# Kernel tuning notes

Measured on AMD Instinct MI355X. Metric: run time of the kernel, lower is better.

Reference implementation:

```python
import jax, jax.numpy as jnp
import numpy as np
from jax import lax

NT, TL = 32, 64           # num_trajs, traj_length
H, W, C = 84, 84, 4       # Atari frame stack
SIZE = 256                # LSTM hidden size
NOUT = 18                 # num_outputs
FEAT = 6 * 6 * 32         # after four stride-2 SAME convs: 84->42->21->11->6
DN = ('NHWC', 'HWIO', 'NHWC')


def setup_inputs() -> dict:
    key = jax.random.key(0)
    ks = jax.random.split(key, 8)
    d = {}
    d['inputs'] = jax.random.normal(ks[0], (NT * TL, H, W, C), jnp.float32)
    cin = C
    for i in range(4):
        d[f'w{i+1}'] = jax.random.normal(ks[1 + i], (3, 3, cin, 32), jnp.float32) * 0.1
        d[f'b{i+1}'] = jnp.zeros((32,), jnp.float32)
        cin = 32
    d['lstm_w'] = jax.random.normal(ks[5], (FEAT + SIZE, 4 * SIZE), jnp.float32) * 0.05
    d['lstm_b'] = jnp.zeros((4 * SIZE,), jnp.float32)
    d['fc_w'] = jax.random.normal(ks[6], (SIZE, NOUT), jnp.float32) * 0.01
    d['fc_b'] = jnp.zeros((NOUT,), jnp.float32)
    d['c0'] = jnp.zeros((NT, SIZE), jnp.float32)
    d['h0'] = jnp.zeros((NT, SIZE), jnp.float32)
    return d


def reference(inputs, w1, b1, w2, b2, w3, b3, w4, b4,
              lstm_w, lstm_b, fc_w, fc_b, c0, h0):
    x = inputs
    for w, b in ((w1, b1), (w2, b2), (w3, b3), (w4, b4)):
        x = jax.nn.elu(lax.conv_general_dilated(
            x, w, window_strides=(2, 2), padding='SAME',
            dimension_numbers=DN) + b)
    # [NT*TL, 6, 6, 32] -> [TL, NT, FEAT] (time-major for scan)
    xs = x.reshape(NT, TL, FEAT).transpose(1, 0, 2)

    def step(carry, xt):
        c, h = carry
        gates = jnp.concatenate([xt, h], axis=-1) @ lstm_w + lstm_b
        i, j, f, o = jnp.split(gates, 4, axis=-1)
        # BasicLSTMCell with forget_bias = 1.0
        new_c = c * jax.nn.sigmoid(f + 1.0) + jax.nn.sigmoid(i) * jnp.tanh(j)
        new_h = jnp.tanh(new_c) * jax.nn.sigmoid(o)
        return (new_c, new_h), new_h

    _, outs = lax.scan(step, (c0, h0), xs)          # outs: [TL, NT, SIZE]
    feats = outs.transpose(1, 0, 2).reshape(-1, SIZE)  # batch-major flatten
    logits = feats @ fc_w + fc_b                    # [NT*TL, NOUT]
    return logits
```

## Files before the change

kernel.cpp:

```cpp
#include <hip/hip_runtime.h>
#include <math.h>

#define NTRAJ 32
#define TLEN  64
#define BATCH (NTRAJ*TLEN)

__device__ __forceinline__ float eluf(float x){ return x > 0.f ? x : expm1f(x); }
__device__ __forceinline__ float sigmf(float x){ return 1.f/(1.f+expf(-x)); }

__global__ __launch_bounds__(256) void conv1_kernel(
    const float* __restrict__ in,
    const float* __restrict__ w,
    const float* __restrict__ b,
    float* __restrict__ out)
{
    int bid = blockIdx.x;
    bid = (bid & 7)*1764 + (bid >> 3);
    int pos = bid*256 + threadIdx.x;
    int n   = pos / (42*42);
    int rem = pos % (42*42);
    int oy  = rem / 42, ox = rem % 42;
    float acc[32];
    #pragma unroll
    for(int o=0;o<32;o++) acc[o] = b[o];
    for(int ky=0; ky<3; ky++){
        int iy = 2*oy + ky;
        if(iy >= 84) continue;
        for(int kx=0; kx<3; kx++){
            int ix = 2*ox + kx;
            if(ix >= 84) continue;
            float4 v = *(const float4*)(in + (((n*84 + iy)*84) + ix)*4);
            const float* wq = w + (ky*3 + kx)*128;
            #pragma unroll
            for(int o=0;o<32;o++) acc[o] += v.x*wq[o];
            #pragma unroll
            for(int o=0;o<32;o++) acc[o] += v.y*wq[32+o];
            #pragma unroll
            for(int o=0;o<32;o++) acc[o] += v.z*wq[64+o];
            #pragma unroll
            for(int o=0;o<32;o++) acc[o] += v.w*wq[96+o];
        }
    }
    float4* op = (float4*)(out + (size_t)pos*32);
    #pragma unroll
    for(int q=0;q<8;q++)
        op[q] = make_float4(eluf(acc[4*q]), eluf(acc[4*q+1]),
                            eluf(acc[4*q+2]), eluf(acc[4*q+3]));
}

template<int IH, int IW, int OH, int OW, int PB>
__global__ __launch_bounds__(256) void convN_kernel(
    const float* __restrict__ in,
    const float* __restrict__ w,
    const float* __restrict__ b,
    float* __restrict__ out)
{
    int bid = blockIdx.x;
    const int cpx = gridDim.x >> 3;
    bid = (bid & 7)*cpx + (bid >> 3);
    int pos = bid*256 + threadIdx.x;
    if(pos >= BATCH*OH*OW) return;
    int n   = pos / (OH*OW);
    int rem = pos % (OH*OW);
    int oy  = rem / OW, ox = rem % OW;
    float acc[32];
    #pragma unroll
    for(int o=0;o<32;o++) acc[o] = b[o];
    for(int ky=0; ky<3; ky++){
        int iy = 2*oy + ky - PB;
        if(iy < 0 || iy >= IH) continue;
        for(int kx=0; kx<3; kx++){
            int ix = 2*ox + kx - PB;
            if(ix < 0 || ix >= IW) continue;
            const float4* ip = (const float4*)(in + ((size_t)(n*IH + iy)*IW + ix)*32);
            const float* wp = w + (ky*3 + kx)*1024;
            #pragma unroll
            for(int c4=0;c4<8;c4++){
                float4 x = ip[c4];
                const float* wq = wp + c4*128;
                #pragma unroll
                for(int o=0;o<32;o++) acc[o] += x.x*wq[o];
                #pragma unroll
                for(int o=0;o<32;o++) acc[o] += x.y*wq[32+o];
                #pragma unroll
                for(int o=0;o<32;o++) acc[o] += x.z*wq[64+o];
                #pragma unroll
                for(int o=0;o<32;o++) acc[o] += x.w*wq[96+o];
            }
        }
    }
    float4* op = (float4*)(out + (size_t)pos*32);
    #pragma unroll
    for(int q=0;q<8;q++)
        op[q] = make_float4(eluf(acc[4*q]), eluf(acc[4*q+1]),
                            eluf(acc[4*q+2]), eluf(acc[4*q+3]));
}

__global__ __launch_bounds__(256) void relayout_kernel(
    const float* __restrict__ p4,
    float* __restrict__ at,
    unsigned long long* __restrict__ hbuf)
{
    int i = blockIdx.x*256 + threadIdx.x;
    if(i < 64*8192) hbuf[i] = 0ull;
    int f = i >> 11, r = i & 2047;
    int tt = r >> 5, n = r & 31;
    int nt = n*64 + tt;
    at[i] = p4[nt*1152 + f];
}

__global__ __launch_bounds__(256) void gx_gemm_kernel(
    const float* __restrict__ at,
    const float* __restrict__ lw,
    const float* __restrict__ lb,
    float* __restrict__ gx)
{
    int lane = threadIdx.x & 63;
    int wv   = threadIdx.x >> 6;
    int r0   = blockIdx.x * 16;
    int oc   = blockIdx.y*256 + wv*64 + lane;
    float acc[16];
    float bias = lb[oc];
    #pragma unroll
    for(int i=0;i<16;i++) acc[i] = bias;
    #pragma unroll 4
    for(int k=0;k<1152;k++){
        float wval = lw[k*1024 + oc];
        const float* ap = at + k*2048 + r0;
        #pragma unroll
        for(int i=0;i<16;i++) acc[i] += ap[i] * wval;
    }
    #pragma unroll
    for(int i=0;i<16;i++) gx[(r0+i)*1024 + oc] = acc[i];
}

__global__ __launch_bounds__(256) void lstm_coop_kernel(
    const float* __restrict__ gx,
    const float* __restrict__ lw,
    const float* __restrict__ c0,
    const float* __restrict__ h0,
    float* __restrict__ feats,
    unsigned long long* __restrict__ hbuf)
{
    __shared__ float hs[32*260];
    __shared__ float wp[16*516];
    __shared__ float gl[32*33];

    const int wg = blockIdx.x;
    const int t  = threadIdx.x;
    const float* wh = lw + 1152*1024;

    for(int i=0;i<32;i++){
        int e = t + 256*i;
        int k = e >> 5, c = e & 31;
        int gc = (c>>3)*256 + wg*8 + (c&7);
        wp[(c>>1)*516 + (k>>1)*4 + (k&1)*2 + (c&1)] = wh[k*1024 + gc];
    }
    const int un = t >> 3, uu = t & 7;
    float cst = c0[un*256 + wg*8 + uu];

    const int np = t >> 4, cp = t & 15;
    const int n0 = 2*np, n1 = 2*np + 1;
    const int c0l = 2*cp, c1l = 2*cp + 1;
    const int g0 = (c0l>>3)*256 + wg*8 + (c0l&7);
    const int g1 = (c1l>>3)*256 + wg*8 + (c1l&7);

    const float4* hs4 = (const float4*)hs;
    const float4* wp4 = (const float4*)wp;
    __syncthreads();

    for(int st=0; st<64; ++st){
        const float* gr0 = gx + (size_t)(st*32 + n0)*1024;
        const float* gr1 = gx + (size_t)(st*32 + n1)*1024;
        float gx00 = gr0[g0], gx01 = gr0[g1];
        float gx10 = gr1[g0], gx11 = gr1[g1];

        if(st == 0){
            const float4* hp4 = (const float4*)h0;
            #pragma unroll
            for(int i=0;i<8;i++){
                int q = t + 256*i;
                int row = q >> 6, col4 = q & 63;
                ((float4*)hs)[row*65 + col4] = hp4[q];
            }
        } else {
            const unsigned long long* src = hbuf + (size_t)(st-1)*8192;
            const unsigned tag = (unsigned)st;
            unsigned long long v[32];
            #pragma unroll
            for(int i=0;i<32;i++)
                v[i] = __hip_atomic_load(&src[i*256 + t],
                    __ATOMIC_RELAXED, __HIP_MEMORY_SCOPE_AGENT);
            unsigned spins = 0;
            for(;;){
                bool ok = true;
                #pragma unroll
                for(int i=0;i<32;i++){
                    if((unsigned)(v[i] >> 32) != tag){
                        v[i] = __hip_atomic_load(&src[i*256 + t],
                            __ATOMIC_RELAXED, __HIP_MEMORY_SCOPE_AGENT);
                        ok = false;
                    }
                }
                if(ok) break;
                __builtin_amdgcn_s_sleep(1);
                if(++spins > (1u<<21)) break;
            }
            #pragma unroll
            for(int i=0;i<32;i++)
                hs[i*260 + t] = __uint_as_float((unsigned)v[i]);
        }
        __syncthreads();

        float a00=0.f, a01=0.f, a10=0.f, a11=0.f;
        const float4* h0r = hs4 + n0*65;
        const float4* h1r = hs4 + n1*65;
        const float4* wr  = wp4 + cp*129;
        #pragma unroll 8
        for(int k4=0;k4<64;k4++){
            float4 A = wr[2*k4], B = wr[2*k4+1];
            float4 x = h0r[k4], y = h1r[k4];
            a00 += x.x*A.x + x.y*A.z + x.z*B.x + x.w*B.z;
            a01 += x.x*A.y + x.y*A.w + x.z*B.y + x.w*B.w;
            a10 += y.x*A.x + y.y*A.z + y.z*B.x + y.w*B.z;
            a11 += y.x*A.y + y.y*A.w + y.z*B.y + y.w*B.w;
        }
        gl[n0*33 + c0l] = a00 + gx00;
        gl[n0*33 + c1l] = a01 + gx01;
        gl[n1*33 + c0l] = a10 + gx10;
        gl[n1*33 + c1l] = a11 + gx11;
        __syncthreads();

        {
            float i_ = gl[un*33 +      uu];
            float j_ = gl[un*33 +  8 + uu];
            float f_ = gl[un*33 + 16 + uu];
            float o_ = gl[un*33 + 24 + uu];
            cst = cst*sigmf(f_ + 1.f) + sigmf(i_)*tanhf(j_);
            float h = tanhf(cst)*sigmf(o_);
            int col = wg*8 + uu;
            feats[(un*64 + st)*256 + col] = h;
            unsigned long long pv =
                ((unsigned long long)(unsigned)(st+1) << 32) |
                (unsigned long long)__float_as_uint(h);
            __hip_atomic_store(&hbuf[(size_t)st*8192 + un*256 + col], pv,
                               __ATOMIC_RELAXED, __HIP_MEMORY_SCOPE_AGENT);
        }
        __syncthreads();
    }
}

__global__ __launch_bounds__(64) void fc_kernel(
    const float* __restrict__ feats, const float* __restrict__ fw,
    const float* __restrict__ fb,    float* __restrict__ out)
{
    __shared__ float h[256];
    int p = blockIdx.x, t = threadIdx.x;
    *(float4*)&h[t*4] = *(const float4*)(feats + p*256 + t*4);
    __syncthreads();
    if(t < 18){
        float acc = fb[t];
        for(int k=0;k<256;k++) acc += h[k]*fw[k*18 + t];
        out[p*18 + t] = acc;
    }
}

extern "C" void kernel_launch(void* const* d_in, const int* in_sizes, int n_in,
                              void* d_out, int out_size, void* d_ws, size_t ws_size,
                              hipStream_t stream) {
    const float* inp = (const float*)d_in[0];
    const float* w1  = (const float*)d_in[1];  const float* b1 = (const float*)d_in[2];
    const float* w2  = (const float*)d_in[3];  const float* b2 = (const float*)d_in[4];
    const float* w3  = (const float*)d_in[5];  const float* b3 = (const float*)d_in[6];
    const float* w4  = (const float*)d_in[7];  const float* b4 = (const float*)d_in[8];
    const float* lw  = (const float*)d_in[9];  const float* lb = (const float*)d_in[10];
    const float* fw  = (const float*)d_in[11]; const float* fb = (const float*)d_in[12];
    const float* c0  = (const float*)d_in[13]; const float* h0 = (const float*)d_in[14];
    float* out = (float*)d_out;
    float* ws  = (float*)d_ws;

    const size_t n1 = (size_t)32*3612672;
    const size_t n3 = (size_t)32*247808;
    const size_t n4 = (size_t)32*73728;

    float* p1 = ws;
    float* p2 = p1 + n1;
    float* p3 = ws;
    float* p4 = p3 + n3;
    float* at = p4 + n4;
    float* gxb   = at  + (size_t)1152*2048;
    float* feats = gxb + (size_t)2048*1024;
    unsigned long long* hbuf =
        (unsigned long long*)(feats + (size_t)2048*256);

    conv1_kernel<<<14112,256,0,stream>>>(inp, w1, b1, p1);
    convN_kernel<42,42,21,21,0><<<3528,256,0,stream>>>(p1, w2, b2, p2);
    convN_kernel<21,21,11,11,1><<<968,256,0,stream>>>(p2, w3, b3, p3);
    convN_kernel<11,11, 6, 6,1><<<288,256,0,stream>>>(p3, w4, b4, p4);
    relayout_kernel<<<9216,256,0,stream>>>(p4, at, hbuf);
    gx_gemm_kernel<<<dim3(128,4),256,0,stream>>>(at, lw, lb, gxb);
    lstm_coop_kernel<<<32,256,0,stream>>>(gxb, lw, c0, h0, feats, hbuf);
    fc_kernel<<<2048,64,0,stream>>>(feats, fw, fb, out);
}
```

Measured before the change: 1.784 ms.

## Stage conv input tiles in shared memory and enlarge gx GEMM row tile

All four conv kernels now load an image row-band (or whole images for the later layers) into shared memory in channel-planar layout once per block. Each thread then reads its 3x3 window from LDS instead of re-reading overlapping input pixels from global memory, so the grids are retiled per image or tile. The gx GEMM now handles 32 rows per block instead of 16, which reuses each weight load more at the cost of extra registers. Risks include lower occupancy from the larger LDS footprint and idle threads in the partially filled tiles.

```diff
diff --git a/kernel.cpp b/kernel.cpp
--- a/kernel.cpp
+++ b/kernel.cpp
@@ -14,86 +14,139 @@
     const float* __restrict__ b,
     float* __restrict__ out)
 {
+    constexpr int IH=84, IW=84, OH=42, OW=42;
+    constexpr int SROWS=25, NPX=SROWS*IW, NPXP=NPX+1;
+    __shared__ float xs[4*NPXP];
     int bid = blockIdx.x;
-    bid = (bid & 7)*1764 + (bid >> 3);
-    int pos = bid*256 + threadIdx.x;
-    int n   = pos / (42*42);
-    int rem = pos % (42*42);
-    int oy  = rem / 42, ox = rem % 42;
-    float acc[32];
-    #pragma unroll
-    for(int o=0;o<32;o++) acc[o] = b[o];
-    for(int ky=0; ky<3; ky++){
-        int iy = 2*oy + ky;
-        if(iy >= 84) continue;
-        for(int kx=0; kx<3; kx++){
-            int ix = 2*ox + kx;
-            if(ix >= 84) continue;
-            float4 v = *(const float4*)(in + (((n*84 + iy)*84) + ix)*4);
-            const float* wq = w + (ky*3 + kx)*128;
-            #pragma unroll
-            for(int o=0;o<32;o++) acc[o] += v.x*wq[o];
-            #pragma unroll
-            for(int o=0;o<32;o++) acc[o] += v.y*wq[32+o];
-            #pragma unroll
-            for(int o=0;o<32;o++) acc[o] += v.z*wq[64+o];
-            #pragma unroll
-            for(int o=0;o<32;o++) acc[o] += v.w*wq[96+o];
-        }
-    }
-    float4* op = (float4*)(out + (size_t)pos*32);
-    #pragma unroll
-    for(int q=0;q<8;q++)
-        op[q] = make_float4(eluf(acc[4*q]), eluf(acc[4*q+1]),
-                            eluf(acc[4*q+2]), eluf(acc[4*q+3]));
-}
-
-template<int IH, int IW, int OH, int OW, int PB>
-__global__ __launch_bounds__(256) void convN_kernel(
+    bid = (bid & 7)*(8192/8) + (bid >> 3);
+    const int img  = bid >> 2;
+    const int tile = bid & 3;
+    const int oy0  = tile*12;
+    const int R    = (tile==3) ? 6 : 12;
+    const int iy0  = 2*oy0;
+    const int rows = min(SROWS, IH - iy0);
+    const int t = threadIdx.x;
+    const float4* gs = (const float4*)(in + (((size_t)img*IH + iy0)*IW)*4);
+    for(int p = t; p < rows*IW; p += 256){
+        float4 v = gs[p];
+        xs[0*NPXP + p] = v.x;  xs[1*NPXP + p] = v.y;
+        xs[2*NPXP + p] = v.z;  xs[3*NPXP + p] = v.w;
+    }
+    __syncthreads();
+    const int npo = R*OW;
+    if(t < 252){
+        for(int h=0; h<2; ++h){
+            int px = t + h*252;
+            if(px >= npo) break;
+            int oy = oy0 + px/OW, ox = px%OW;
+            float acc[32];
+            #pragma unroll
+            for(int o=0;o<32;o++) acc[o] = b[o];
+            for(int ky=0;ky<3;ky++){
+                int iy = 2*oy + ky;
+                if(iy >= IH) continue;
+                int rb = (iy - iy0)*IW;
+                for(int kx=0;kx<3;kx++){
+                    int ix = 2*ox + kx;
+                    if(ix >= IW) continue;
+                    const float* wq = w + (ky*3 + kx)*128;
+                    float x0 = xs[0*NPXP + rb + ix];
+                    float x1 = xs[1*NPXP + rb + ix];
+                    float x2 = xs[2*NPXP + rb + ix];
+                    float x3 = xs[3*NPXP + rb + ix];
+                    #pragma unroll
+                    for(int o=0;o<32;o++) acc[o] += x0*wq[o];
+                    #pragma unroll
+                    for(int o=0;o<32;o++) acc[o] += x1*wq[32+o];
+                    #pragma unroll
+                    for(int o=0;o<32;o++) acc[o] += x2*wq[64+o];
+                    #pragma unroll
+                    for(int o=0;o<32;o++) acc[o] += x3*wq[96+o];
+                }
+            }
+            float4* op = (float4*)(out + ((size_t)(img*OH + oy)*OW + ox)*32);
+            #pragma unroll
+            for(int q=0;q<8;q++)
+                op[q] = make_float4(eluf(acc[4*q]), eluf(acc[4*q+1]),
+                                    eluf(acc[4*q+2]), eluf(acc[4*q+3]));
+        }
+    }
+}
+
+template<int IH,int IW,int OH,int OW,int PB,int NIMG,int OROWS,int NTILES>
+__global__ __launch_bounds__(256) void convT_kernel(
     const float* __restrict__ in,
     const float* __restrict__ w,
     const float* __restrict__ b,
     float* __restrict__ out)
 {
+    constexpr int SROWS = (NTILES==1) ? IH : (2*OROWS+1);
+    constexpr int NPX   = NIMG*SROWS*IW;
+    constexpr int NPXP  = NPX + ((NPX&1) ? 0 : 1);
+    __shared__ float xs[32*NPXP];
     int bid = blockIdx.x;
-    const int cpx = gridDim.x >> 3;
-    bid = (bid & 7)*cpx + (bid >> 3);
-    int pos = bid*256 + threadIdx.x;
-    if(pos >= BATCH*OH*OW) return;
-    int n   = pos / (OH*OW);
-    int rem = pos % (OH*OW);
-    int oy  = rem / OW, ox = rem % OW;
-    float acc[32];
-    #pragma unroll
-    for(int o=0;o<32;o++) acc[o] = b[o];
-    for(int ky=0; ky<3; ky++){
-        int iy = 2*oy + ky - PB;
-        if(iy < 0 || iy >= IH) continue;
-        for(int kx=0; kx<3; kx++){
-            int ix = 2*ox + kx - PB;
-            if(ix < 0 || ix >= IW) continue;
-            const float4* ip = (const float4*)(in + ((size_t)(n*IH + iy)*IW + ix)*32);
-            const float* wp = w + (ky*3 + kx)*1024;
-            #pragma unroll
-            for(int c4=0;c4<8;c4++){
-                float4 x = ip[c4];
-                const float* wq = wp + c4*128;
-                #pragma unroll
-                for(int o=0;o<32;o++) acc[o] += x.x*wq[o];
-                #pragma unroll
-                for(int o=0;o<32;o++) acc[o] += x.y*wq[32+o];
-                #pragma unroll
-                for(int o=0;o<32;o++) acc[o] += x.z*wq[64+o];
-                #pragma unroll
-                for(int o=0;o<32;o++) acc[o] += x.w*wq[96+o];
+    bid = (bid & 7)*(gridDim.x >> 3) + (bid >> 3);
+    const int img0 = (bid / NTILES)*NIMG;
+    const int tile = bid % NTILES;
+    const int oy0  = tile*OROWS;
+    const int R    = min(OROWS, OH - oy0);
+    const int iy0  = (NTILES==1) ? 0 : 2*oy0;
+    const int rows = min(SROWS, IH - iy0);
+    const int t = threadIdx.x;
+    for(int il=0; il<NIMG; ++il){
+        const float4* gs = (const float4*)(in + (((size_t)(img0+il)*IH + iy0)*IW)*32);
+        const int ne = rows*IW*8;
+        for(int e=t; e<ne; e+=256){
+            int px = e >> 3, c4 = e & 7;
+            float4 v = gs[e];
+            int bb = il*(SROWS*IW) + px;
+            xs[(c4*4+0)*NPXP + bb] = v.x;
+            xs[(c4*4+1)*NPXP + bb] = v.y;
+            xs[(c4*4+2)*NPXP + bb] = v.z;
+            xs[(c4*4+3)*NPXP + bb] = v.w;
+        }
+    }
+    __syncthreads();
+    const int npo = NIMG*R*OW;
+    if(t < npo){
+        const int il  = t/(R*OW);
+        const int rem = t%(R*OW);
+        const int oy  = oy0 + rem/OW;
+        const int ox  = rem%OW;
+        float acc[32];
+        #pragma unroll
+        for(int o=0;o<32;o++) acc[o] = b[o];
+        for(int ky=0;ky<3;ky++){
+            int iy = 2*oy + ky - PB;
+            if(iy < iy0 || iy >= IH) continue;
+            for(int kx=0;kx<3;kx++){
+                int ix = 2*ox + kx - PB;
+                if(ix < 0 || ix >= IW) continue;
+                int base = il*(SROWS*IW) + (iy-iy0)*IW + ix;
+                const float* wp = w + (ky*3 + kx)*1024;
+                for(int ci=0;ci<32;ci+=4){
+                    float x0 = xs[(ci+0)*NPXP + base];
+                    float x1 = xs[(ci+1)*NPXP + base];
+                    float x2 = xs[(ci+2)*NPXP + base];
+                    float x3 = xs[(ci+3)*NPXP + base];
+                    const float* wq = wp + ci*32;
+                    #pragma unroll
+                    for(int o=0;o<32;o++) acc[o] += x0*wq[o];
+                    #pragma unroll
+                    for(int o=0;o<32;o++) acc[o] += x1*wq[32+o];
+                    #pragma unroll
+                    for(int o=0;o<32;o++) acc[o] += x2*wq[64+o];
+                    #pragma unroll
+                    for(int o=0;o<32;o++) acc[o] += x3*wq[96+o];
+                }
             }
         }
-    }
-    float4* op = (float4*)(out + (size_t)pos*32);
-    #pragma unroll
-    for(int q=0;q<8;q++)
-        op[q] = make_float4(eluf(acc[4*q]), eluf(acc[4*q+1]),
-                            eluf(acc[4*q+2]), eluf(acc[4*q+3]));
+        float4* op = (float4*)(out + ((size_t)((img0+il)*OH + oy)*OW + ox)*32);
+        #pragma unroll
+        for(int q=0;q<8;q++)
+            op[q] = make_float4(eluf(acc[4*q]), eluf(acc[4*q+1]),
+                                eluf(acc[4*q+2]), eluf(acc[4*q+3]));
+    }
 }
 
 __global__ __launch_bounds__(256) void relayout_kernel(
@@ -117,21 +170,21 @@
 {
     int lane = threadIdx.x & 63;
     int wv   = threadIdx.x >> 6;
-    int r0   = blockIdx.x * 16;
+    int r0   = blockIdx.x * 32;
     int oc   = blockIdx.y*256 + wv*64 + lane;
-    float acc[16];
+    float acc[32];
     float bias = lb[oc];
     #pragma unroll
-    for(int i=0;i<16;i++) acc[i] = bias;
-    #pragma unroll 4
+    for(int i=0;i<32;i++) acc[i] = bias;
+    #pragma unroll 2
     for(int k=0;k<1152;k++){
         float wval = lw[k*1024 + oc];
         const float* ap = at + k*2048 + r0;
         #pragma unroll
-        for(int i=0;i<16;i++) acc[i] += ap[i] * wval;
+        for(int i=0;i<32;i++) acc[i] += ap[i] * wval;
     }
     #pragma unroll
-    for(int i=0;i<16;i++) gx[(r0+i)*1024 + oc] = acc[i];
+    for(int i=0;i<32;i++) gx[(r0+i)*1024 + oc] = acc[i];
 }
 
 __global__ __launch_bounds__(256) void lstm_coop_kernel(
@@ -293,12 +346,12 @@
     unsigned long long* hbuf =
         (unsigned long long*)(feats + (size_t)2048*256);
 
-    conv1_kernel<<<14112,256,0,stream>>>(inp, w1, b1, p1);
-    convN_kernel<42,42,21,21,0><<<3528,256,0,stream>>>(p1, w2, b2, p2);
-    convN_kernel<21,21,11,11,1><<<968,256,0,stream>>>(p2, w3, b3, p3);
-    convN_kernel<11,11, 6, 6,1><<<288,256,0,stream>>>(p3, w4, b4, p4);
+    conv1_kernel<<<8192,256,0,stream>>>(inp, w1, b1, p1);
+    convT_kernel<42,42,21,21,0,1, 6,4><<<8192,256,0,stream>>>(p1, w2, b2, p2);
+    convT_kernel<21,21,11,11,1,1,11,1><<<2048,256,0,stream>>>(p2, w3, b3, p3);
+    convT_kernel<11,11, 6, 6,1,4, 6,1><<< 512,256,0,stream>>>(p3, w4, b4, p4);
     relayout_kernel<<<9216,256,0,stream>>>(p4, at, hbuf);
-    gx_gemm_kernel<<<dim3(128,4),256,0,stream>>>(at, lw, lb, gxb);
+    gx_gemm_kernel<<<dim3(64,4),256,0,stream>>>(at, lw, lb, gxb);
     lstm_coop_kernel<<<32,256,0,stream>>>(gxb, lw, c0, h0, feats, hbuf);
     fc_kernel<<<2048,64,0,stream>>>(feats, fw, fb, out);
 }
```

Result: slower. 2.423 ms (+35.8%).

## Compute two adjacent output pixels per thread in conv kernels, widen GEMM tile

Applied to the files above, without the earlier changes.

Each conv thread now computes two horizontally adjacent output pixels. It loads a 5-wide input row strip once, so the overlapping input column is reused and each weight load feeds two FMAs. This halves weight-load traffic per FMA and cuts grid sizes, at the cost of doubled accumulator registers and possibly lower occupancy. The gx GEMM also processes 32 rows per block instead of 16 to reuse each weight value more.

```diff
diff --git a/kernel.cpp b/kernel.cpp
--- a/kernel.cpp
+++ b/kernel.cpp
@@ -14,86 +14,113 @@
     const float* __restrict__ b,
     float* __restrict__ out)
 {
+    constexpr int IH=84, IW=84, OH=42, OW=42, PPR=21;
     int bid = blockIdx.x;
-    bid = (bid & 7)*1764 + (bid >> 3);
+    bid = (bid & 7)*882 + (bid >> 3);
     int pos = bid*256 + threadIdx.x;
-    int n   = pos / (42*42);
-    int rem = pos % (42*42);
-    int oy  = rem / 42, ox = rem % 42;
-    float acc[32];
-    #pragma unroll
-    for(int o=0;o<32;o++) acc[o] = b[o];
+    int n   = pos / (OH*PPR);
+    int rem = pos % (OH*PPR);
+    int oy  = rem / PPR;
+    int ox0 = 2*(rem % PPR);
+    float acc0[32], acc1[32];
+    #pragma unroll
+    for(int o=0;o<32;o++){ acc0[o] = b[o]; acc1[o] = b[o]; }
+    const int ix0 = 2*ox0;
     for(int ky=0; ky<3; ky++){
         int iy = 2*oy + ky;
-        if(iy >= 84) continue;
-        for(int kx=0; kx<3; kx++){
-            int ix = 2*ox + kx;
-            if(ix >= 84) continue;
-            float4 v = *(const float4*)(in + (((n*84 + iy)*84) + ix)*4);
-            const float* wq = w + (ky*3 + kx)*128;
-            #pragma unroll
-            for(int o=0;o<32;o++) acc[o] += v.x*wq[o];
-            #pragma unroll
-            for(int o=0;o<32;o++) acc[o] += v.y*wq[32+o];
-            #pragma unroll
-            for(int o=0;o<32;o++) acc[o] += v.z*wq[64+o];
-            #pragma unroll
-            for(int o=0;o<32;o++) acc[o] += v.w*wq[96+o];
-        }
-    }
-    float4* op = (float4*)(out + (size_t)pos*32);
+        if(iy >= IH) continue;
+        const float* rowp = in + ((size_t)(n*IH + iy)*IW)*4;
+        float4 xc[5];
+        #pragma unroll
+        for(int j=0;j<5;j++){
+            int ixc = ix0 + j;
+            xc[j] = (ixc < IW) ? *(const float4*)(rowp + ixc*4)
+                               : make_float4(0.f,0.f,0.f,0.f);
+        }
+        #pragma unroll
+        for(int kx=0;kx<3;kx++){
+            const float* wk = w + (ky*3 + kx)*128;
+            const float* xa = (const float*)&xc[kx];
+            const float* xb = (const float*)&xc[kx+2];
+            #pragma unroll
+            for(int e=0;e<4;e++){
+                float a_ = xa[e], b_ = xb[e];
+                const float* wo = wk + e*32;
+                #pragma unroll
+                for(int o=0;o<32;o++){ acc0[o] += a_*wo[o]; acc1[o] += b_*wo[o]; }
+            }
+        }
+    }
+    float4* op = (float4*)(out + ((size_t)(n*OH + oy)*OW + ox0)*32);
     #pragma unroll
     for(int q=0;q<8;q++)
-        op[q] = make_float4(eluf(acc[4*q]), eluf(acc[4*q+1]),
-                            eluf(acc[4*q+2]), eluf(acc[4*q+3]));
-}
-
-template<int IH, int IW, int OH, int OW, int PB>
-__global__ __launch_bounds__(256) void convN_kernel(
+        op[q] = make_float4(eluf(acc0[4*q]), eluf(acc0[4*q+1]),
+                            eluf(acc0[4*q+2]), eluf(acc0[4*q+3]));
+    #pragma unroll
+    for(int q=0;q<8;q++)
+        op[8+q] = make_float4(eluf(acc1[4*q]), eluf(acc1[4*q+1]),
+                              eluf(acc1[4*q+2]), eluf(acc1[4*q+3]));
+}
+
+template<int IH,int IW,int OH,int OW,int PB>
+__global__ __launch_bounds__(256) void convP_kernel(
     const float* __restrict__ in,
     const float* __restrict__ w,
     const float* __restrict__ b,
     float* __restrict__ out)
 {
+    constexpr int PPR = (OW+1)/2;
     int bid = blockIdx.x;
-    const int cpx = gridDim.x >> 3;
-    bid = (bid & 7)*cpx + (bid >> 3);
+    bid = (bid & 7)*(gridDim.x >> 3) + (bid >> 3);
     int pos = bid*256 + threadIdx.x;
-    if(pos >= BATCH*OH*OW) return;
-    int n   = pos / (OH*OW);
-    int rem = pos % (OH*OW);
-    int oy  = rem / OW, ox = rem % OW;
-    float acc[32];
-    #pragma unroll
-    for(int o=0;o<32;o++) acc[o] = b[o];
+    int n   = pos / (OH*PPR);
+    int rem = pos % (OH*PPR);
+    int oy  = rem / PPR;
+    int ox0 = 2*(rem % PPR);
+    const bool p1v = (ox0+1) < OW;
+    float acc0[32], acc1[32];
+    #pragma unroll
+    for(int o=0;o<32;o++){ acc0[o] = b[o]; acc1[o] = b[o]; }
+    const int ix0 = 2*ox0 - PB;
     for(int ky=0; ky<3; ky++){
         int iy = 2*oy + ky - PB;
-        if(iy < 0 || iy >= IH) continue;
-        for(int kx=0; kx<3; kx++){
-            int ix = 2*ox + kx - PB;
-            if(ix < 0 || ix >= IW) continue;
-            const float4* ip = (const float4*)(in + ((size_t)(n*IH + iy)*IW + ix)*32);
-            const float* wp = w + (ky*3 + kx)*1024;
-            #pragma unroll
-            for(int c4=0;c4<8;c4++){
-                float4 x = ip[c4];
-                const float* wq = wp + c4*128;
+        if((unsigned)iy >= (unsigned)IH) continue;
+        const float* rowp = in + ((size_t)(n*IH + iy)*IW)*32;
+        for(int ci4=0; ci4<8; ci4++){
+            float4 xc[5];
+            #pragma unroll
+            for(int j=0;j<5;j++){
+                int ixc = ix0 + j;
+                xc[j] = ((unsigned)ixc < (unsigned)IW)
+                      ? *(const float4*)(rowp + ixc*32 + ci4*4)
+                      : make_float4(0.f,0.f,0.f,0.f);
+            }
+            #pragma unroll
+            for(int kx=0;kx<3;kx++){
+                const float* wk = w + (ky*3 + kx)*1024 + ci4*128;
+                const float* xa = (const float*)&xc[kx];
+                const float* xb = (const float*)&xc[kx+2];
                 #pragma unroll
-                for(int o=0;o<32;o++) acc[o] += x.x*wq[o];
-                #pragma unroll
-                for(int o=0;o<32;o++) acc[o] += x.y*wq[32+o];
-                #pragma unroll
-                for(int o=0;o<32;o++) acc[o] += x.z*wq[64+o];
-                #pragma unroll
-                for(int o=0;o<32;o++) acc[o] += x.w*wq[96+o];
-            }
-        }
-    }
-    float4* op = (float4*)(out + (size_t)pos*32);
+                for(int e=0;e<4;e++){
+                    float a_ = xa[e], b_ = xb[e];
+                    const float* wo = wk + e*32;
+                    #pragma unroll
+                    for(int o=0;o<32;o++){ acc0[o] += a_*wo[o]; acc1[o] += b_*wo[o]; }
+                }
+            }
+        }
+    }
+    float4* op = (float4*)(out + ((size_t)(n*OH + oy)*OW + ox0)*32);
     #pragma unroll
     for(int q=0;q<8;q++)
-        op[q] = make_float4(eluf(acc[4*q]), eluf(acc[4*q+1]),
-                            eluf(acc[4*q+2]), eluf(acc[4*q+3]));
+        op[q] = make_float4(eluf(acc0[4*q]), eluf(acc0[4*q+1]),
+                            eluf(acc0[4*q+2]), eluf(acc0[4*q+3]));
+    if(p1v){
+        #pragma unroll
+        for(int q=0;q<8;q++)
+            op[8+q] = make_float4(eluf(acc1[4*q]), eluf(acc1[4*q+1]),
+                                  eluf(acc1[4*q+2]), eluf(acc1[4*q+3]));
+    }
 }
 
 __global__ __launch_bounds__(256) void relayout_kernel(
@@ -117,21 +144,21 @@
 {
     int lane = threadIdx.x & 63;
     int wv   = threadIdx.x >> 6;
-    int r0   = blockIdx.x * 16;
+    int r0   = blockIdx.x * 32;
     int oc   = blockIdx.y*256 + wv*64 + lane;
-    float acc[16];
+    float acc[32];
     float bias = lb[oc];
     #pragma unroll
-    for(int i=0;i<16;i++) acc[i] = bias;
-    #pragma unroll 4
+    for(int i=0;i<32;i++) acc[i] = bias;
+    #pragma unroll 2
     for(int k=0;k<1152;k++){
         float wval = lw[k*1024 + oc];
         const float* ap = at + k*2048 + r0;
         #pragma unroll
-        for(int i=0;i<16;i++) acc[i] += ap[i] * wval;
-    }
-    #pragma unroll
-    for(int i=0;i<16;i++) gx[(r0+i)*1024 + oc] = acc[i];
+        for(int i=0;i<32;i++) acc[i] += ap[i] * wval;
+    }
+    #pragma unroll
+    for(int i=0;i<32;i++) gx[(r0+i)*1024 + oc] = acc[i];
 }
 
 __global__ __launch_bounds__(256) void lstm_coop_kernel(
@@ -293,12 +320,12 @@
     unsigned long long* hbuf =
         (unsigned long long*)(feats + (size_t)2048*256);
 
-    conv1_kernel<<<14112,256,0,stream>>>(inp, w1, b1, p1);
-    convN_kernel<42,42,21,21,0><<<3528,256,0,stream>>>(p1, w2, b2, p2);
-    convN_kernel<21,21,11,11,1><<<968,256,0,stream>>>(p2, w3, b3, p3);
-    convN_kernel<11,11, 6, 6,1><<<288,256,0,stream>>>(p3, w4, b4, p4);
+    conv1_kernel<<<7056,256,0,stream>>>(inp, w1, b1, p1);
+    convP_kernel<42,42,21,21,0><<<1848,256,0,stream>>>(p1, w2, b2, p2);
+    convP_kernel<21,21,11,11,1><<< 528,256,0,stream>>>(p2, w3, b3, p3);
+    convP_kernel<11,11, 6, 6,1><<< 144,256,0,stream>>>(p3, w4, b4, p4);
     relayout_kernel<<<9216,256,0,stream>>>(p4, at, hbuf);
-    gx_gemm_kernel<<<dim3(128,4),256,0,stream>>>(at, lw, lb, gxb);
+    gx_gemm_kernel<<<dim3(64,4),256,0,stream>>>(at, lw, lb, gxb);
     lstm_coop_kernel<<<32,256,0,stream>>>(gxb, lw, c0, h0, feats, hbuf);
     fc_kernel<<<2048,64,0,stream>>>(feats, fw, fb, out);
 }
```

New measurement: 2.493 ms. 39.8% more time.
